# Kernel optimization log

Hardware: AMD Instinct MI355X
Metric: run time of the kernel (lower is better)

Reference implementation:

```python
import jax, jax.numpy as jnp
import numpy as np

B, S, D, H = 2, 2048, 1024, 16
DEPTH = D // H

def setup_inputs() -> dict:
    key = jax.random.key(0)
    ks = jax.random.split(key, 11)
    def glorot(k, shape):
        lim = np.sqrt(6.0 / (shape[0] + shape[1]))
        return jax.random.uniform(k, shape, jnp.float32, -lim, lim)
    return {
        'q': jax.random.normal(ks[0], (B, S, D), jnp.float32),
        'k': jax.random.normal(ks[1], (B, S, D), jnp.float32),
        'v': jax.random.normal(ks[2], (B, S, D), jnp.float32),
        'wq': glorot(ks[3], (D, D)), 'bq': jnp.zeros((D,), jnp.float32),
        'wk': glorot(ks[4], (D, D)), 'bk': jnp.zeros((D,), jnp.float32),
        'wv': glorot(ks[5], (D, D)), 'bv': jnp.zeros((D,), jnp.float32),
        'wo': glorot(ks[6], (D, D)), 'bo': jnp.zeros((D,), jnp.float32),
    }

def _split_heads(x):
    # [B,S,D] -> [B,H,S,depth]
    return x.reshape(B, S, H, DEPTH).transpose(0, 2, 1, 3)

def reference(q, k, v, wq, bq, wk, bk, wv, bv, wo, bo):
    qh = _split_heads(q @ wq + bq)
    kh = _split_heads(k @ wk + bk)
    vh = _split_heads(v @ wv + bv)
    scale = 1.0 / jnp.sqrt(jnp.float32(DEPTH))
    scores = jnp.einsum('bhqd,bhkd->bhqk', qh, kh) * scale
    attn = jax.nn.softmax(scores, axis=-1)
    out = jnp.einsum('bhqk,bhkd->bhqd', attn, vh)  # [B,H,S,depth]
    out = out.transpose(0, 2, 1, 3).reshape(B, S, D)
    return out @ wo + bo
```

## Files before the change

kernel.cpp:

```cpp
#include <hip/hip_runtime.h>
#include <hip/hip_bf16.h>
#include <stdint.h>

#define Bb 2
#define Ss 2048
#define Dd 1024
#define Hh 16

typedef __hip_bfloat16 bf16;
typedef __attribute__((ext_vector_type(8))) short bf16x8;
typedef __attribute__((ext_vector_type(4))) short short4v;
typedef __attribute__((ext_vector_type(4))) float f32x4;
typedef __attribute__((ext_vector_type(4))) unsigned uint4v;
typedef __attribute__((ext_vector_type(2))) unsigned uint2v;

__device__ __forceinline__ void gl_lds16(const void* g, void* l) {
  __builtin_amdgcn_global_load_lds((const __attribute__((address_space(1))) void*)g,
                                   (__attribute__((address_space(3))) void*)l, 16, 0, 0);
}

__device__ __forceinline__ unsigned pack2(float a, float b) {
  unsigned ua = __builtin_bit_cast(unsigned, a), ub = __builtin_bit_cast(unsigned, b);
  return ((ua + 0x8000u) >> 16) | ((ub + 0x8000u) & 0xffff0000u);
}

__device__ __forceinline__ bf16x8 lds_frag(const char* base, int row, int cl) {
  int phys = cl ^ (row & 7);
  return *(const bf16x8*)(base + row * 128 + phys * 16);
}

__global__ void convert_qk(const float* __restrict__ q, const float* __restrict__ k,
                           bf16* __restrict__ Qb, bf16* __restrict__ Kb) {
  int sel = blockIdx.x >> 11;
  const float* src = sel ? k : q;
  bf16* dst = sel ? Kb : Qb;
  size_t i = (size_t)(blockIdx.x & 2047) * 256 + threadIdx.x;
  f32x4 v0 = *(const f32x4*)(src + i * 8);
  f32x4 v1 = *(const f32x4*)(src + i * 8 + 4);
  uint4v o = {pack2(v0[0], v0[1]), pack2(v0[2], v0[3]),
              pack2(v1[0], v1[1]), pack2(v1[2], v1[3])};
  *(uint4v*)((char*)dst + i * 16) = o;
}

__global__ void transpose_w4(const float* w0, const float* w1, const float* w2, const float* w3,
                             bf16* t0, bf16* t1, bf16* t2, bf16* t3) {
  const float* W;
  bf16* T;
  switch (blockIdx.z) {
    case 0: W = w0; T = t0; break;
    case 1: W = w1; T = t1; break;
    case 2: W = w2; T = t2; break;
    default: W = w3; T = t3; break;
  }
  __shared__ bf16 tile[64][65];
  int tx = threadIdx.x, ty = threadIdx.y;
  int r0 = blockIdx.y * 64, c0 = blockIdx.x * 64;
#pragma unroll
  for (int j = 0; j < 16; j++) {
    int r = ty + j * 4;
    tile[r][tx] = __float2bfloat16(W[(size_t)(r0 + r) * 1024 + c0 + tx]);
  }
  __syncthreads();
#pragma unroll
  for (int j = 0; j < 16; j++) {
    int r = ty + j * 4;
    T[(size_t)(c0 + r) * 1024 + r0 + tx] = tile[tx][r];
  }
}

#define SCL 0.180336878f
__global__ __launch_bounds__(256, 3) void gemm_qkv(
    const bf16* __restrict__ Qb, const bf16* __restrict__ Kb, const float* __restrict__ v,
    const bf16* __restrict__ WTall,
    const float* __restrict__ bq, const float* __restrict__ bk, const float* __restrict__ bv,
    bf16* __restrict__ Qp, bf16* __restrict__ Kp, bf16* __restrict__ Vt) {
  __shared__ char As[128 * 128], Bs[128 * 128];
  const int K = 1024;
  int tid = threadIdx.x, lane = tid & 63, w = tid >> 6;
  int quad = lane >> 4, l16 = lane & 15;
  int xcd = blockIdx.x & 7, slot = blockIdx.x >> 3;
  int pair = xcd * 12 + (slot % 12);
  int nloc_blk = slot / 12;
  int mblk = pair / 3, sel = pair % 3;
  int m0 = mblk * 128;
  int nloc0 = nloc_blk * 128;
  int n0 = sel * 1024 + nloc0;
  const bf16* Ab = (sel == 0) ? Qb : Kb;
  const float* bias = (sel == 0) ? bq : (sel == 1) ? bk : bv;
  int wm = (w >> 1) * 64, wn = (w & 1) * 64;
  f32x4 acc[4][4] = {};
  for (int k0 = 0; k0 < K; k0 += 64) {
    __syncthreads();
    if (sel < 2) {
#pragma unroll
      for (int i = 0; i < 4; i++) {
        int c = i * 256 + tid;
        int row = c >> 3, cc = c & 7;
        int g = (cc ^ (row & 7)) * 16;
        gl_lds16((const char*)Ab + ((size_t)(m0 + row) * K + k0) * 2 + g, As + c * 16);
        gl_lds16((const char*)WTall + ((size_t)(n0 + row) * K + k0) * 2 + g, Bs + c * 16);
      }
    } else {
#pragma unroll
      for (int i = 0; i < 4; i++) {
        int c = i * 256 + tid;
        int row = c >> 3, cc = c & 7;
        int g = cc ^ (row & 7);
        const float* src = v + (size_t)(m0 + row) * K + k0 + g * 8;
        f32x4 v0 = *(const f32x4*)src;
        f32x4 v1 = *(const f32x4*)(src + 4);
        uint4v o = {pack2(v0[0], v0[1]), pack2(v0[2], v0[3]),
                    pack2(v1[0], v1[1]), pack2(v1[2], v1[3])};
        *(uint4v*)(As + c * 16) = o;
        gl_lds16((const char*)WTall + ((size_t)(n0 + row) * K + k0) * 2 + g * 16, Bs + c * 16);
      }
    }
    __syncthreads();
#pragma unroll
    for (int ks = 0; ks < 2; ks++) {
      bf16x8 a[4], b[4];
#pragma unroll
      for (int mt = 0; mt < 4; mt++) a[mt] = lds_frag(As, wm + mt * 16 + l16, ks * 4 + quad);
#pragma unroll
      for (int nt = 0; nt < 4; nt++) b[nt] = lds_frag(Bs, wn + nt * 16 + l16, ks * 4 + quad);
#pragma unroll
      for (int mt = 0; mt < 4; mt++)
#pragma unroll
        for (int nt = 0; nt < 4; nt++)
          acc[mt][nt] = __builtin_amdgcn_mfma_f32_16x16x32_bf16(a[mt], b[nt], acc[mt][nt], 0, 0, 0);
    }
  }
#pragma unroll
  for (int nt = 0; nt < 4; nt++) {
    int nloc = nloc0 + wn + nt * 16 + l16;
    float bvv = bias[nloc];
#pragma unroll
    for (int mt = 0; mt < 4; mt++) {
      int row = m0 + wm + mt * 16 + quad * 4;
      if (sel == 2) {
        int d = nloc & 63, h = nloc >> 6;
        int b_ = row >> 11, s = row & 2047;
        int bh = b_ * 16 + h;
        float f0 = acc[mt][nt][0] + bvv, f1 = acc[mt][nt][1] + bvv;
        float f2 = acc[mt][nt][2] + bvv, f3 = acc[mt][nt][3] + bvv;
        uint2v pv = {pack2(f0, f1), pack2(f2, f3)};
        *(uint2v*)((char*)Vt + ((size_t)(bh * 64 + d) * Ss + s) * 2) = pv;
      } else {
        bf16* C = (sel == 0) ? Qp : Kp;
        float scale = (sel == 0) ? SCL : 1.0f;
#pragma unroll
        for (int r = 0; r < 4; r++)
          C[(size_t)(row + r) * 1024 + nloc] = __float2bfloat16((acc[mt][nt][r] + bvv) * scale);
      }
    }
  }
}

__global__ __launch_bounds__(512, 4) void flash_attn(
    const bf16* __restrict__ Q, const bf16* __restrict__ Kp,
    const bf16* __restrict__ Vt, bf16* __restrict__ O) {
  __shared__ char lds[48 * 1024];
  int tid = threadIdx.x, lane = tid & 63, w = tid >> 6;
  int quad = lane >> 4, l16 = lane & 15;
  int bx = blockIdx.x;
  int bh = bx & 31, b = bh >> 4, h = bh & 15;
  int q0 = (bx >> 5) * 128;
  int qw = (w & 3) * 32;
  int parity = w >> 2;
  const char* Ksb = lds + 16 * 1024 + parity * 16 * 1024;
  const char* Vsb = Ksb + 8 * 1024;

#pragma unroll
  for (int i = 0; i < 2; i++) {
    int c = i * 512 + tid;
    int row = c >> 3, cc = c & 7;
    int gcol = (cc ^ (row & 7)) * 16;
    gl_lds16((const char*)Q + ((size_t)(b * Ss + q0 + row) * Dd + h * 64) * 2 + gcol, lds + c * 16);
  }

  f32x4 o_acc[2][4] = {};
  f32x4 l_acc[2] = {};
  const short4v ones4 = {(short)0x3F80, (short)0x3F80, (short)0x3F80, (short)0x3F80};

  for (int kb0 = 0; kb0 < Ss / 64; kb0 += 2) {
    __syncthreads();
    {
      int row = tid >> 3, cc = tid & 7;
      int gcol = (cc ^ (row & 7)) * 16;
#pragma unroll
      for (int i = 0; i < 4; i++) {
        int kbb = kb0 + (i >> 1);
        char* dst = lds + 16 * 1024 + i * 8 * 1024 + tid * 16;
        if ((i & 1) == 0)
          gl_lds16((const char*)Kp + ((size_t)(b * Ss + kbb * 64 + row) * Dd + h * 64) * 2 + gcol, dst);
        else
          gl_lds16((const char*)Vt + ((size_t)(bh * 64 + row) * Ss + kbb * 64) * 2 + gcol, dst);
      }
    }
    __syncthreads();

    f32x4 s[4][2] = {};
#pragma unroll
    for (int ks = 0; ks < 2; ks++) {
      bf16x8 ak[4], bq[2];
#pragma unroll
      for (int kt = 0; kt < 4; kt++) ak[kt] = lds_frag(Ksb, kt * 16 + l16, ks * 4 + quad);
#pragma unroll
      for (int qt = 0; qt < 2; qt++) bq[qt] = lds_frag(lds, qw + qt * 16 + l16, ks * 4 + quad);
#pragma unroll
      for (int kt = 0; kt < 4; kt++)
#pragma unroll
        for (int qt = 0; qt < 2; qt++)
          s[kt][qt] = __builtin_amdgcn_mfma_f32_16x16x32_bf16(ak[kt], bq[qt], s[kt][qt], 0, 0, 0);
    }

#pragma unroll
    for (int kt = 0; kt < 4; kt++) {
      short4v af[2];
#pragma unroll
      for (int qt = 0; qt < 2; qt++) {
        union { short4v s4; uint2v u2; } u;
        u.u2[0] = pack2(exp2f(s[kt][qt][0]), exp2f(s[kt][qt][1]));
        u.u2[1] = pack2(exp2f(s[kt][qt][2]), exp2f(s[kt][qt][3]));
        af[qt] = u.s4;
      }
#pragma unroll
      for (int nt = 0; nt < 4; nt++) {
        int row = nt * 16 + l16;
        int chunk = kt * 2 + (quad >> 1);
        int addr = row * 128 + ((chunk ^ (row & 7)) * 16) + (quad & 1) * 8;
        short4v bfv = *(const short4v*)(Vsb + addr);
#pragma unroll
        for (int qt = 0; qt < 2; qt++)
          o_acc[qt][nt] = __builtin_amdgcn_mfma_f32_16x16x16bf16_1k(af[qt], bfv, o_acc[qt][nt], 0, 0, 0);
      }
#pragma unroll
      for (int qt = 0; qt < 2; qt++)
        l_acc[qt] = __builtin_amdgcn_mfma_f32_16x16x16bf16_1k(af[qt], ones4, l_acc[qt], 0, 0, 0);
    }
  }

  __syncthreads();
  float* Obuf = (float*)lds;
  float* Lbuf = (float*)(lds + 32 * 1024);
  if (parity == 1) {
#pragma unroll
    for (int qt = 0; qt < 2; qt++)
#pragma unroll
      for (int r = 0; r < 4; r++) {
        int qrow = qw + qt * 16 + quad * 4 + r;
#pragma unroll
        for (int nt = 0; nt < 4; nt++) Obuf[qrow * 64 + nt * 16 + l16] = o_acc[qt][nt][r];
        Lbuf[qrow] = l_acc[qt][r];
      }
  }
  __syncthreads();
  if (parity == 0) {
#pragma unroll
    for (int qt = 0; qt < 2; qt++)
#pragma unroll
      for (int r = 0; r < 4; r++) {
        int qrow = qw + qt * 16 + quad * 4 + r;
        float inv = 1.0f / (l_acc[qt][r] + Lbuf[qrow]);
        int grow = b * Ss + q0 + qrow;
#pragma unroll
        for (int nt = 0; nt < 4; nt++) {
          float val = (o_acc[qt][nt][r] + Obuf[qrow * 64 + nt * 16 + l16]) * inv;
          O[(size_t)grow * Dd + h * 64 + nt * 16 + l16] = __float2bfloat16(val);
        }
      }
  }
}

__global__ __launch_bounds__(256, 4) void gemm_out(
    const bf16* __restrict__ AO, const bf16* __restrict__ WT,
    const float* __restrict__ bo, float* __restrict__ out) {
  __shared__ char As[64 * 128], Bs[64 * 128];
  const int K = 1024;
  int tid = threadIdx.x, lane = tid & 63, w = tid >> 6;
  int quad = lane >> 4, l16 = lane & 15;
  int xcd = blockIdx.x & 7, slot = blockIdx.x >> 3;
  int mblk = xcd * 8 + (slot & 7);
  int nblk = slot >> 3;
  int m0 = mblk * 64, n0 = nblk * 64;
  int wm = (w & 1) * 32, wn = (w >> 1) * 32;
  f32x4 acc[2][2] = {};
  for (int k0 = 0; k0 < K; k0 += 64) {
    __syncthreads();
#pragma unroll
    for (int i = 0; i < 2; i++) {
      int c = i * 256 + tid;
      int row = c >> 3, cc = c & 7;
      int g = (cc ^ (row & 7)) * 16;
      gl_lds16((const char*)AO + ((size_t)(m0 + row) * K + k0) * 2 + g, As + c * 16);
      gl_lds16((const char*)WT + ((size_t)(n0 + row) * K + k0) * 2 + g, Bs + c * 16);
    }
    __syncthreads();
#pragma unroll
    for (int ks = 0; ks < 2; ks++) {
      bf16x8 a[2], b[2];
#pragma unroll
      for (int mt = 0; mt < 2; mt++) a[mt] = lds_frag(As, wm + mt * 16 + l16, ks * 4 + quad);
#pragma unroll
      for (int nt = 0; nt < 2; nt++) b[nt] = lds_frag(Bs, wn + nt * 16 + l16, ks * 4 + quad);
#pragma unroll
      for (int mt = 0; mt < 2; mt++)
#pragma unroll
        for (int nt = 0; nt < 2; nt++)
          acc[mt][nt] = __builtin_amdgcn_mfma_f32_16x16x32_bf16(a[mt], b[nt], acc[mt][nt], 0, 0, 0);
    }
  }
#pragma unroll
  for (int nt = 0; nt < 2; nt++) {
    int col = n0 + wn + nt * 16 + l16;
    float bvv = bo[col];
#pragma unroll
    for (int mt = 0; mt < 2; mt++) {
      int row = m0 + wm + mt * 16 + quad * 4;
#pragma unroll
      for (int r = 0; r < 4; r++)
        out[(size_t)(row + r) * 1024 + col] = acc[mt][nt][r] + bvv;
    }
  }
}

extern "C" void kernel_launch(void* const* d_in, const int* in_sizes, int n_in,
                              void* d_out, int out_size, void* d_ws, size_t ws_size,
                              hipStream_t stream) {
  const float* q  = (const float*)d_in[0];
  const float* k  = (const float*)d_in[1];
  const float* v  = (const float*)d_in[2];
  const float* wq = (const float*)d_in[3];
  const float* bq = (const float*)d_in[4];
  const float* wk = (const float*)d_in[5];
  const float* bk = (const float*)d_in[6];
  const float* wv = (const float*)d_in[7];
  const float* bv = (const float*)d_in[8];
  const float* wo = (const float*)d_in[9];
  const float* bo = (const float*)d_in[10];
  float* out = (float*)d_out;

  char* ws = (char*)d_ws;
  const size_t MB = (size_t)1024 * 1024;
  bf16* wtall = (bf16*)(ws + 0 * MB);
  bf16* wtq = wtall;
  bf16* wtk = (bf16*)(ws + 2 * MB);
  bf16* wtv = (bf16*)(ws + 4 * MB);
  bf16* wto = (bf16*)(ws + 6 * MB);
  bf16* Qp  = (bf16*)(ws + 8 * MB);
  bf16* AO  = Qp;
  bf16* Kp  = (bf16*)(ws + 16 * MB);
  bf16* Vt  = (bf16*)(ws + 24 * MB);
  bf16* Qb  = (bf16*)((char*)d_out + 0 * MB);
  bf16* Kb  = (bf16*)((char*)d_out + 8 * MB);

  dim3 tb(64, 4);
  convert_qk<<<4096, 256, 0, stream>>>(q, k, Qb, Kb);
  transpose_w4<<<dim3(16, 16, 4), tb, 0, stream>>>(wq, wk, wv, wo, wtq, wtk, wtv, wto);
  gemm_qkv<<<768, 256, 0, stream>>>(Qb, Kb, v, wtall, bq, bk, bv, Qp, Kp, Vt);
  flash_attn<<<512, 512, 0, stream>>>(Qp, Kp, Vt, AO);
  gemm_out<<<1024, 256, 0, stream>>>(AO, wto, bo, out);
}
```

Baseline: 250.0 us.

## Double-buffer K/V tiles in flash attention and keep Q fragments in registers

```diff
diff --git a/kernel.cpp b/kernel.cpp
--- a/kernel.cpp
+++ b/kernel.cpp
@@ -22,6 +22,12 @@
 __device__ __forceinline__ unsigned pack2(float a, float b) {
   unsigned ua = __builtin_bit_cast(unsigned, a), ub = __builtin_bit_cast(unsigned, b);
   return ((ua + 0x8000u) >> 16) | ((ub + 0x8000u) & 0xffff0000u);
+}
+
+__device__ __forceinline__ unsigned cvtpk2(float a, float b) {
+  unsigned r;
+  asm("v_cvt_pk_bf16_f32 %0, %1, %2" : "=v"(r) : "v"(a), "v"(b));
+  return r;
 }
 
 __device__ __forceinline__ bf16x8 lds_frag(const char* base, int row, int cl) {
@@ -159,7 +165,7 @@
 __global__ __launch_bounds__(512, 4) void flash_attn(
     const bf16* __restrict__ Q, const bf16* __restrict__ Kp,
     const bf16* __restrict__ Vt, bf16* __restrict__ O) {
-  __shared__ char lds[48 * 1024];
+  __shared__ char lds[64 * 1024];
   int tid = threadIdx.x, lane = tid & 63, w = tid >> 6;
   int quad = lane >> 4, l16 = lane & 15;
   int bx = blockIdx.x;
@@ -167,51 +173,66 @@
   int q0 = (bx >> 5) * 128;
   int qw = (w & 3) * 32;
   int parity = w >> 2;
-  const char* Ksb = lds + 16 * 1024 + parity * 16 * 1024;
-  const char* Vsb = Ksb + 8 * 1024;
-
-#pragma unroll
-  for (int i = 0; i < 2; i++) {
-    int c = i * 512 + tid;
-    int row = c >> 3, cc = c & 7;
+
+  auto stage = [&](int dsel, int kb0) {
+    int row = tid >> 3, cc = tid & 7;
     int gcol = (cc ^ (row & 7)) * 16;
-    gl_lds16((const char*)Q + ((size_t)(b * Ss + q0 + row) * Dd + h * 64) * 2 + gcol, lds + c * 16);
-  }
+#pragma unroll
+    for (int i = 0; i < 4; i++) {
+      int kbb = kb0 + (i >> 1);
+      char* dst = lds + dsel * 32 * 1024 + i * 8 * 1024 + tid * 16;
+      if ((i & 1) == 0)
+        gl_lds16((const char*)Kp + ((size_t)(b * Ss + kbb * 64 + row) * Dd + h * 64) * 2 + gcol, dst);
+      else
+        gl_lds16((const char*)Vt + ((size_t)(bh * 64 + row) * Ss + kbb * 64) * 2 + gcol, dst);
+    }
+  };
+
+  stage(0, 0);
+  asm volatile("" ::: "memory");
+
+  bf16x8 qf[2][2];
+#pragma unroll
+  for (int qt = 0; qt < 2; qt++)
+#pragma unroll
+    for (int ks = 0; ks < 2; ks++) {
+      int qrow = q0 + qw + qt * 16 + l16;
+      qf[qt][ks] = *(const bf16x8*)((const char*)Q +
+          ((size_t)(b * Ss + qrow) * Dd + h * 64 + (ks * 4 + quad) * 8) * 2);
+    }
 
   f32x4 o_acc[2][4] = {};
   f32x4 l_acc[2] = {};
   const short4v ones4 = {(short)0x3F80, (short)0x3F80, (short)0x3F80, (short)0x3F80};
 
-  for (int kb0 = 0; kb0 < Ss / 64; kb0 += 2) {
-    __syncthreads();
-    {
-      int row = tid >> 3, cc = tid & 7;
-      int gcol = (cc ^ (row & 7)) * 16;
-#pragma unroll
-      for (int i = 0; i < 4; i++) {
-        int kbb = kb0 + (i >> 1);
-        char* dst = lds + 16 * 1024 + i * 8 * 1024 + tid * 16;
-        if ((i & 1) == 0)
-          gl_lds16((const char*)Kp + ((size_t)(b * Ss + kbb * 64 + row) * Dd + h * 64) * 2 + gcol, dst);
-        else
-          gl_lds16((const char*)Vt + ((size_t)(bh * 64 + row) * Ss + kbb * 64) * 2 + gcol, dst);
-      }
-    }
-    __syncthreads();
+  const int NT = Ss / 128;
+  for (int it = 0; it < NT; ++it) {
+    int cur = it & 1;
+    if (it < NT - 1) {
+      stage(cur ^ 1, (it + 1) * 2);
+      asm volatile("s_waitcnt vmcnt(4)" ::: "memory");
+    } else {
+      asm volatile("s_waitcnt vmcnt(0)" ::: "memory");
+    }
+    __builtin_amdgcn_s_barrier();
+    asm volatile("" ::: "memory");
+
+    const char* Ksb = lds + cur * 32 * 1024 + parity * 16 * 1024;
+    const char* Vsb = Ksb + 8 * 1024;
 
     f32x4 s[4][2] = {};
 #pragma unroll
     for (int ks = 0; ks < 2; ks++) {
-      bf16x8 ak[4], bq[2];
+      bf16x8 ak[4];
 #pragma unroll
       for (int kt = 0; kt < 4; kt++) ak[kt] = lds_frag(Ksb, kt * 16 + l16, ks * 4 + quad);
-#pragma unroll
-      for (int qt = 0; qt < 2; qt++) bq[qt] = lds_frag(lds, qw + qt * 16 + l16, ks * 4 + quad);
+      __builtin_amdgcn_s_setprio(1);
 #pragma unroll
       for (int kt = 0; kt < 4; kt++)
 #pragma unroll
         for (int qt = 0; qt < 2; qt++)
-          s[kt][qt] = __builtin_amdgcn_mfma_f32_16x16x32_bf16(ak[kt], bq[qt], s[kt][qt], 0, 0, 0);
+          s[kt][qt] = __builtin_amdgcn_mfma_f32_16x16x32_bf16(ak[kt], qf[qt][ks], s[kt][qt], 0, 0, 0);
+      __builtin_amdgcn_s_setprio(0);
     }
 
 #pragma unroll
@@ -220,10 +241,11 @@
 #pragma unroll
       for (int qt = 0; qt < 2; qt++) {
         union { short4v s4; uint2v u2; } u;
-        u.u2[0] = pack2(exp2f(s[kt][qt][0]), exp2f(s[kt][qt][1]));
-        u.u2[1] = pack2(exp2f(s[kt][qt][2]), exp2f(s[kt][qt][3]));
+        u.u2[0] = cvtpk2(exp2f(s[kt][qt][0]), exp2f(s[kt][qt][1]));
+        u.u2[1] = cvtpk2(exp2f(s[kt][qt][2]), exp2f(s[kt][qt][3]));
         af[qt] = u.s4;
       }
+      __builtin_amdgcn_s_setprio(1);
 #pragma unroll
       for (int nt = 0; nt < 4; nt++) {
         int row = nt * 16 + l16;
@@ -237,7 +259,11 @@
 #pragma unroll
       for (int qt = 0; qt < 2; qt++)
         l_acc[qt] = __builtin_amdgcn_mfma_f32_16x16x16bf16_1k(af[qt], ones4, l_acc[qt], 0, 0, 0);
-    }
+      __builtin_amdgcn_s_setprio(0);
+    }
+
+    asm volatile("" ::: "memory");
+    __builtin_amdgcn_s_barrier();
   }
 
   __syncthreads();
```

Measured after the change: 266.8 us. 1.07x slower.
